# Optimization experiments

Measured on AMD Instinct MI355X. Metric: run time of the kernel, lower is better.

The kernel has to match this reference:

```python
import jax, jax.numpy as jnp
import numpy as np

TIME_GAP_BUCKETS = 64
B, L, H, MAX_T = 256, 200, 256, 256
VOCAB, N_GROUPS = 50000, 16
EPS = 1e-5


def setup_inputs() -> dict:
    key = jax.random.key(0)
    ks = jax.random.split(key, 16)
    lengths = jax.random.randint(ks[0], (B,), 0, L + 1)
    mask = jnp.arange(L)[None, :] < lengths[:, None]

    def toks(k, hi):  # jagged padded-dense: zeros past each row's length
        return jnp.where(mask, jax.random.randint(k, (B, L), 0, hi), 0)

    inp = {
        'history_tokens': toks(ks[1], VOCAB),
        'history_post_tokens': toks(ks[2], VOCAB),
        'history_author_tokens': toks(ks[3], VOCAB),
        'history_action_tokens': toks(ks[4], VOCAB),
        'history_time_gap': toks(ks[5], TIME_GAP_BUCKETS + 1),
        'history_group_ids': jnp.where(mask, jnp.sort(jax.random.randint(ks[6], (B, L), 1, N_GROUPS + 1), axis=1), 0),
        'lengths': lengths,
    }
    s = 0.02
    inp['token_emb'] = jax.random.normal(ks[7], (VOCAB, H)) * s
    inp['ln_gamma'] = jnp.ones((6 * H,))
    inp['ln_beta'] = jnp.zeros((6 * H,))
    inp['w1'] = jax.random.normal(ks[8], (6 * H, 4 * H)) * (1.0 / np.sqrt(6 * H)).astype(np.float32)
    inp['b1'] = jnp.zeros((4 * H,))
    inp['w2'] = jax.random.normal(ks[9], (4 * H, H)) * (1.0 / np.sqrt(4 * H)).astype(np.float32)
    inp['b2'] = jnp.zeros((H,))
    inp['time_gap_emb'] = (jax.random.normal(ks[10], (TIME_GAP_BUCKETS + 1, H)) * s).at[0].set(0.0)  # padding_idx=0
    inp['group_emb'] = (jax.random.normal(ks[11], (N_GROUPS + 1, H)) * s).at[0].set(0.0)  # padding_idx=0
    inp['pos_emb'] = jax.random.normal(ks[12], (MAX_T, H)) * s
    inp['sep_token'] = jax.random.normal(ks[13], (H,)) * 0.02
    return inp


def _layernorm(x, g, b):
    mu = jnp.mean(x, axis=-1, keepdims=True)
    var = jnp.mean(jnp.square(x - mu), axis=-1, keepdims=True)
    return (x - mu) * jax.lax.rsqrt(var + EPS) * g + b


def _merge_with_sep(event_tokens, group_ids, mask, sep_token):
    # mask is a prefix mask (positions < lengths), so valid tokens are contiguous.
    Bn, Ln, Hn = event_tokens.shape
    next_mask = jnp.pad(mask[:, 1:], ((0, 0), (0, 1)))
    next_group = jnp.pad(group_ids[:, 1:], ((0, 0), (0, 1)))
    sep_after = mask & next_mask & (group_ids != next_group)  # insert sep after token i
    seps_before = jnp.cumsum(sep_after, axis=1) - sep_after.astype(jnp.int32)  # exclusive scan
    token_pos = jnp.arange(Ln)[None, :] + seps_before  # position within merged piece list
    total = mask.sum(axis=1) + sep_after.sum(axis=1)  # [B] merged piece count
    offset = MAX_T - total  # right-align; negative -> leading pieces dropped
    tok_idx = offset[:, None] + token_pos
    sep_idx = tok_idx + 1
    tok_idx = jnp.where(mask & (tok_idx >= 0), tok_idx, MAX_T)  # MAX_T => dropped
    sep_idx = jnp.where(sep_after & (sep_idx >= 0), sep_idx, MAX_T)
    sep_rows = jnp.broadcast_to(sep_token, (Ln, Hn))

    def scatter_one(ev, ti, si):
        buf = jnp.zeros((MAX_T, Hn), ev.dtype)
        buf = buf.at[ti].set(ev, mode='drop')
        buf = buf.at[si].set(sep_rows, mode='drop')
        return buf

    merged = jax.vmap(scatter_one)(event_tokens, tok_idx, sep_idx)
    merged_len = jnp.minimum(total, MAX_T)
    merged_mask = jnp.arange(MAX_T)[None, :] >= (MAX_T - merged_len)[:, None]
    return merged, merged_mask


def reference(history_tokens, history_post_tokens, history_author_tokens,
              history_action_tokens, history_time_gap, history_group_ids,
              lengths, token_emb, ln_gamma, ln_beta, w1, b1, w2, b2,
              time_gap_emb, group_emb, pos_emb, sep_token):
    mask = jnp.arange(L)[None, :] < lengths[:, None]
    hh = token_emb[history_tokens]
    ph = token_emb[history_post_tokens]
    ah = token_emb[history_author_tokens]
    ch = token_emb[history_action_tokens]
    th = time_gap_emb[jnp.clip(history_time_gap, 0, TIME_GAP_BUCKETS)]
    gh = group_emb[history_group_ids]
    ev = jnp.concatenate([hh, ph, ah, ch, th, gh], axis=-1)  # [B, L, 6H]
    x = _layernorm(ev, ln_gamma, ln_beta)
    x = jax.nn.silu(x @ w1 + b1)  # dropout is identity in eval mode
    event_tokens = x @ w2 + b2  # [B, L, H]
    merged, mm = _merge_with_sep(event_tokens, history_group_ids, mask, sep_token)
    merged = (merged + pos_emb[None]) * mm[..., None].astype(merged.dtype)
    return merged, mm
```

## Files before the change

### kernel.cpp

```cpp
#include <hip/hip_runtime.h>
#include <hip/hip_bf16.h>
#include <math.h>

#define B_    256
#define L_    200
#define H_    256
#define MAXT  256
#define SIXH  1536
#define FOURH 1024
#define NPOS  (B_ * L_)

typedef __attribute__((ext_vector_type(8))) short short8;
typedef __attribute__((ext_vector_type(4))) float f32x4;

typedef __attribute__((address_space(3))) void lds_void;
typedef const __attribute__((address_space(1))) void gbl_void;

#define ASM_BAR() asm volatile("s_barrier" ::: "memory")
#define VMCNT3()  asm volatile("s_waitcnt vmcnt(3)" ::: "memory")
#define VMCNT0()  asm volatile("s_waitcnt vmcnt(0)" ::: "memory")

__global__ void scan_offsets(const int* __restrict__ lengths,
                             int* __restrict__ offsets) {
  int t = threadIdx.x;
  int lane = t & 63, wv = t >> 6;
  int len = lengths[t];
  int s = len;
#pragma unroll
  for (int o = 1; o < 64; o <<= 1) {
    int v = __shfl_up(s, o);
    if (lane >= o) s += v;
  }
  __shared__ int wsum[4];
  if (lane == 63) wsum[wv] = s;
  __syncthreads();
  int pre = 0;
#pragma unroll
  for (int k = 0; k < 4; k++)
    if (k < wv) pre += wsum[k];
  s += pre;
  offsets[t] = s - len;
  if (t == 255) offsets[B_] = s;
}

__global__ void zero_pad_x(__hip_bfloat16* __restrict__ x,
                           const int* __restrict__ offsets) {
  int total = offsets[B_];
  int padded = (total + 255) & ~255;
  int row = total + blockIdx.x;
  if (row >= padded) return;
  int t = threadIdx.x;
#pragma unroll
  for (int j = 0; j < 6; j++)
    x[(size_t)row * SIXH + j * 256 + t] = __float2bfloat16(0.0f);
}

__global__ void tpos_kernel(const int* __restrict__ gids,
                            const int* __restrict__ lengths,
                            const int* __restrict__ offsets,
                            int* __restrict__ tpos) {
  int b = blockIdx.x, t = threadIdx.x;
  __shared__ int g[L_];
  int len = lengths[b];
  for (int l = t; l < len; l += 64) g[l] = gids[b * L_ + l];
  __syncthreads();
  if (t != 0) return;
  int base = offsets[b];
  int nsep = 0;
  for (int l = 0; l + 1 < len; l++)
    if (g[l] != g[l + 1]) nsep++;
  int total = len + nsep;
  int off = MAXT - total;
  int sb = 0;
  for (int l = 0; l < len; l++) {
    int ti = off + l + sb;
    tpos[base + l] = (ti >= 0) ? (b * MAXT + ti) : -1;
    if (l + 1 < len && g[l] != g[l + 1]) sb++;
  }
}

__global__ void transpose_both(const float* __restrict__ w1,
                               __hip_bfloat16* __restrict__ w1t,
                               const float* __restrict__ w2,
                               __hip_bfloat16* __restrict__ w2t) {
  __shared__ float tile[32][33];
  int id = blockIdx.x;
  const float* in; __hip_bfloat16* out; int R, C, tc, tr;
  if (id < 1536) {
    in = w1; out = w1t; R = 1536; C = 1024; tc = id & 31; tr = id >> 5;
  } else {
    int j = id - 1536;
    in = w2; out = w2t; R = 1024; C = 256; tc = j & 7; tr = j >> 3;
  }
  int tx = threadIdx.x & 31, ty = threadIdx.x >> 5;
#pragma unroll
  for (int i = 0; i < 4; i++)
    tile[ty + i * 8][tx] = in[(size_t)(tr * 32 + ty + i * 8) * C + tc * 32 + tx];
  __syncthreads();
#pragma unroll
  for (int i = 0; i < 4; i++)
    out[(size_t)(tc * 32 + ty + i * 8) * R + tr * 32 + tx] =
        __float2bfloat16(tile[tx][ty + i * 8]);
}

__global__ void embed_ln_kernel(const int* __restrict__ tok0,
                                const int* __restrict__ tok1,
                                const int* __restrict__ tok2,
                                const int* __restrict__ tok3,
                                const int* __restrict__ tgap,
                                const int* __restrict__ gid,
                                const int* __restrict__ lengths,
                                const int* __restrict__ offsets,
                                const float* __restrict__ token_emb,
                                const float* __restrict__ tg_emb,
                                const float* __restrict__ g_emb,
                                const float* __restrict__ gamma,
                                const float* __restrict__ beta,
                                __hip_bfloat16* __restrict__ xout) {
  int l = blockIdx.x, b = blockIdx.y;
  if (l >= lengths[b]) return;
  int pos = b * L_ + l;
  int row = offsets[b] + l;
  int t = threadIdx.x;
  int wv = t >> 6;
  int ln = t & 63;
  int c4 = ln * 4;

  const float* tab;
  int idx;
  if (wv == 0)      { tab = token_emb; idx = tok0[pos]; }
  else if (wv == 1) { tab = token_emb; idx = tok1[pos]; }
  else if (wv == 2) { tab = token_emb; idx = tok2[pos]; }
  else if (wv == 3) { tab = token_emb; idx = tok3[pos]; }
  else if (wv == 4) { tab = tg_emb;    idx = min(max(tgap[pos], 0), 64); }
  else              { tab = g_emb;     idx = gid[pos]; }

  float4 v = *(const float4*)&tab[(size_t)idx * H_ + c4];

  float s = v.x + v.y + v.z + v.w;
  float q = v.x * v.x + v.y * v.y + v.z * v.z + v.w * v.w;
#pragma unroll
  for (int o = 32; o; o >>= 1) { s += __shfl_down(s, o); q += __shfl_down(q, o); }
  __shared__ float ps[6], pq[6];
  if (ln == 0) { ps[wv] = s; pq[wv] = q; }
  __syncthreads();
  float ts = 0.f, tq = 0.f;
#pragma unroll
  for (int k = 0; k < 6; k++) { ts += ps[k]; tq += pq[k]; }
  float mu = ts * (1.0f / 1536.0f);
  float var = tq * (1.0f / 1536.0f) - mu * mu;
  float rstd = rsqrtf(var + 1e-5f);

  int cbase = wv * 256 + c4;
  float4 gm = *(const float4*)&gamma[cbase];
  float4 bt = *(const float4*)&beta[cbase];
  float y0 = (v.x - mu) * rstd * gm.x + bt.x;
  float y1 = (v.y - mu) * rstd * gm.y + bt.y;
  float y2 = (v.z - mu) * rstd * gm.z + bt.z;
  float y3 = (v.w - mu) * rstd * gm.w + bt.w;
  __hip_bfloat16 h0 = __float2bfloat16(y0), h1 = __float2bfloat16(y1);
  __hip_bfloat16 h2 = __float2bfloat16(y2), h3 = __float2bfloat16(y3);
  ushort4 pk;
  pk.x = *(unsigned short*)&h0; pk.y = *(unsigned short*)&h1;
  pk.z = *(unsigned short*)&h2; pk.w = *(unsigned short*)&h3;
  *(ushort4*)&xout[(size_t)row * SIXH + cbase] = pk;
}

__global__ __launch_bounds__(512, 4)
void gemm1_bk32(const __hip_bfloat16* __restrict__ A,
                const __hip_bfloat16* __restrict__ Bt,
                const float* __restrict__ bias,
                __hip_bfloat16* __restrict__ out,
                const int* __restrict__ total_ptr) {
  constexpr int K = SIXH;
  constexpr int NS = K / 32;
  constexpr int N = FOURH;

  __shared__ __align__(16) char lds[49152];

  int total = total_ptr[0];
  int padded = (total + 255) & ~255;
  int num_mt = padded >> 8;

  int flat = blockIdx.y * 8 + blockIdx.x;
  int xcd = flat & 7;
  int j = flat >> 3;
  int nt = j & 7;
  int mt = (j >> 3) * 8 + xcd;
  if (mt >= num_mt) return;
  int m0 = mt * 256;
  int n0 = nt * 128;

  int tid = threadIdx.x;
  int lane = tid & 63;
  int w = tid >> 6;
  int wave_m = w >> 1;
  int wave_n = w & 1;

  int r15 = lane & 15, g = lane >> 4;
  int slot_r = (((r15 & 1) << 2) | g) ^ (r15 >> 1);
  int lane_off = (r15 >> 1) * 128 + slot_r * 16;

  int s0 = (tid & 7) ^ ((tid >> 3) & 7);
  int scol = (s0 & 3) * 8;
  int row0 = ((tid >> 3) << 1) + (s0 >> 2);

  float bv4[4];
#pragma unroll
  for (int ni = 0; ni < 4; ni++)
    bv4[ni] = bias[n0 + wave_n * 64 + ni * 16 + r15];

#define AREG(d) (lds + (d) * 16384)
#define BREG(d) (lds + 32768 + (d) * 8192)

#define STAGE_A(ks, d)                                                         \
  do {                                                                         \
    __builtin_amdgcn_global_load_lds(                                          \
        (gbl_void*)(A + (size_t)(m0 + row0) * K + (ks) * 32 + scol),           \
        (lds_void*)(AREG(d) + (size_t)tid * 16 % 8192 + 0 * 8192 +             \
                    (tid * 16 / 8192) * 0),                                    \
        16, 0, 0);                                                             \
  } while (0)
#undef STAGE_A
#define STAGE_A(ks, d)                                                         \
  do {                                                                         \
    __builtin_amdgcn_global_load_lds(                                          \
        (gbl_void*)(A + (size_t)(m0 + row0) * K + (ks) * 32 + scol),           \
        (lds_void*)(AREG(d) + w * 1024), 16, 0, 0);                            \
    __builtin_amdgcn_global_load_lds(                                          \
        (gbl_void*)(A + (size_t)(m0 + row0 + 128) * K + (ks) * 32 + scol),     \
        (lds_void*)(AREG(d) + 8192 + w * 1024), 16, 0, 0);                     \
  } while (0)
#define STAGE_B(ks, d)                                                         \
  __builtin_amdgcn_global_load_lds(                                            \
      (gbl_void*)(Bt + (size_t)(n0 + row0) * K + (ks) * 32 + scol),            \
      (lds_void*)(BREG(d) + w * 1024), 16, 0, 0)

  f32x4 acc[4][4] = {};

  STAGE_A(0, 0); STAGE_B(0, 0);
  STAGE_A(1, 1); STAGE_B(1, 1);
  VMCNT3();
  ASM_BAR();

  for (int ks = 0; ks < NS; ++ks) {
    int d = ks & 1;
    int kn = (ks + 2 < NS) ? ks + 2 : NS - 1;
    char* Ad = AREG(d);
    char* Bd = BREG(d);

    short8 a[4], b[4];
#pragma unroll
    for (int ni = 0; ni < 4; ni++)
      b[ni] = *(const short8*)(Bd + (wave_n * 64 + ni * 16) * 64 + lane_off);
#pragma unroll
    for (int mi = 0; mi < 4; mi++)
      a[mi] = *(const short8*)(Ad + (wave_m * 64 + mi * 16) * 64 + lane_off);
    ASM_BAR();

    STAGE_A(kn, d); STAGE_B(kn, d);

    __builtin_amdgcn_s_setprio(1);
#pragma unroll
    for (int mi = 0; mi < 4; mi++)
#pragma unroll
      for (int ni = 0; ni < 4; ni++)
        acc[mi][ni] = __builtin_amdgcn_mfma_f32_16x16x32_bf16(a[mi], b[ni],
                                                              acc[mi][ni], 0, 0, 0);
    __builtin_amdgcn_s_setprio(0);

    VMCNT3();
    ASM_BAR();
  }
  VMCNT0();

  int r0 = g * 4;
#pragma unroll
  for (int mi = 0; mi < 4; mi++)
#pragma unroll
    for (int ni = 0; ni < 4; ni++) {
      int col = n0 + wave_n * 64 + ni * 16 + r15;
      float bv = bv4[ni];
#pragma unroll
      for (int r = 0; r < 4; r++) {
        int row = m0 + wave_m * 64 + mi * 16 + r0 + r;
        float v = acc[mi][ni][r] + bv;
        v = v / (1.0f + __expf(-v));
        out[(size_t)row * N + col] = __float2bfloat16(v);
      }
    }
#undef STAGE_A
#undef STAGE_B
#undef AREG
#undef BREG
}

__global__ void gemm2_scatter(const __hip_bfloat16* __restrict__ A,
                              const __hip_bfloat16* __restrict__ Bt,
                              const float* __restrict__ bias,
                              const int* __restrict__ tpos,
                              const float* __restrict__ pos_emb,
                              float* __restrict__ out,
                              const int* __restrict__ total_ptr,
                              int N, int K) {
  int m0 = blockIdx.y * 128;
  int total = total_ptr[0];
  int padded = (total + 127) & ~127;
  if (m0 >= padded) return;

  __shared__ __hip_bfloat16 As[128 * 64];
  __shared__ __hip_bfloat16 Bs[128 * 64];
  int n0 = blockIdx.x * 128;
  int tid = threadIdx.x;
  int lane = tid & 63, wid = tid >> 6;
  int wm = (wid >> 1) * 64, wn = (wid & 1) * 64;

  int srow = (lane >> 3);
  int scol = (lane & 7) * 8;

  f32x4 acc[4][4] = {};

  for (int k0 = 0; k0 < K; k0 += 64) {
#pragma unroll
    for (int i = 0; i < 4; i++) {
      int c = wid * 4 + i;
      int row = c * 8 + srow;
      __builtin_amdgcn_global_load_lds(
          (gbl_void*)&A[(size_t)(m0 + row) * K + k0 + scol],
          (lds_void*)(As + c * 512), 16, 0, 0);
      __builtin_amdgcn_global_load_lds(
          (gbl_void*)&Bt[(size_t)(n0 + row) * K + k0 + scol],
          (lds_void*)(Bs + c * 512), 16, 0, 0);
    }
    __syncthreads();
#pragma unroll
    for (int kk = 0; kk < 64; kk += 32) {
      short8 a[4], bb[4];
#pragma unroll
      for (int m = 0; m < 4; m++)
        a[m] = *(const short8*)&As[(wm + m * 16 + (lane & 15)) * 64 + kk +
                                   8 * (lane >> 4)];
#pragma unroll
      for (int n = 0; n < 4; n++)
        bb[n] = *(const short8*)&Bs[(wn + n * 16 + (lane & 15)) * 64 + kk +
                                    8 * (lane >> 4)];
#pragma unroll
      for (int m = 0; m < 4; m++)
#pragma unroll
        for (int n = 0; n < 4; n++)
          acc[m][n] = __builtin_amdgcn_mfma_f32_16x16x32_bf16(a[m], bb[n],
                                                              acc[m][n], 0, 0, 0);
    }
    __syncthreads();
  }

  int r0 = (lane >> 4) * 4;
  int cc = lane & 15;
#pragma unroll
  for (int m = 0; m < 4; m++) {
#pragma unroll
    for (int r = 0; r < 4; r++) {
      int row = m0 + wm + m * 16 + r0 + r;
      if (row >= total) continue;
      int pa = tpos[row];
      if (pa < 0) continue;
      int p = pa & (MAXT - 1);
#pragma unroll
      for (int n = 0; n < 4; n++) {
        int col = n0 + wn + n * 16 + cc;
        float v = acc[m][n][r] + bias[col] + pos_emb[p * H_ + col];
        out[(size_t)pa * H_ + col] = v;
      }
    }
  }
}

__global__ void merge2_kernel(const int* __restrict__ gids,
                              const int* __restrict__ lengths,
                              const float* __restrict__ sep_token,
                              const float* __restrict__ pos_emb,
                              float* __restrict__ out) {
  int b = blockIdx.x, t = threadIdx.x;
  __shared__ signed char src[MAXT];
  __shared__ int g[L_];
  __shared__ int sh_total;
  int len = lengths[b];
  src[t] = 0;
  for (int l = t; l < len; l += 256) g[l] = gids[b * L_ + l];
  __syncthreads();
  if (t == 0) {
    int nsep = 0;
    for (int l = 0; l + 1 < len; l++)
      if (g[l] != g[l + 1]) nsep++;
    int total = len + nsep;
    sh_total = total;
    int off = MAXT - total;
    int sb = 0;
    for (int l = 0; l < len; l++) {
      int ti = off + l + sb;
      if (ti >= 0) src[ti] = 2;
      if (l + 1 < len && g[l] != g[l + 1]) {
        if (ti + 1 >= 0) src[ti + 1] = 1;
        sb++;
      }
    }
  }
  __syncthreads();
  int total = sh_total;
  int mlen = min(total, MAXT);

  int q = t >> 6, lane = t & 63, c4 = lane * 4;
  float4 sep4 = *(const float4*)&sep_token[c4];
  float* orow = out + (size_t)b * MAXT * H_;
  for (int p0 = 0; p0 < MAXT; p0 += 4) {
    int p = p0 + q;
    int s = src[p];
    if (s == 2) continue;
    float4 v;
    if (s == 1) {
      float4 pe = *(const float4*)&pos_emb[p * H_ + c4];
      v.x = sep4.x + pe.x; v.y = sep4.y + pe.y;
      v.z = sep4.z + pe.z; v.w = sep4.w + pe.w;
    } else {
      v.x = 0.f; v.y = 0.f; v.z = 0.f; v.w = 0.f;
    }
    *(float4*)&orow[(size_t)p * H_ + c4] = v;
  }
  float* mm = out + (size_t)B_ * MAXT * H_;
  mm[b * MAXT + t] = (t >= MAXT - mlen) ? 1.0f : 0.0f;
}

extern "C" void kernel_launch(void* const* d_in, const int* in_sizes, int n_in,
                              void* d_out, int out_size, void* d_ws,
                              size_t ws_size, hipStream_t stream) {
  const int* tok0 = (const int*)d_in[0];
  const int* tok1 = (const int*)d_in[1];
  const int* tok2 = (const int*)d_in[2];
  const int* tok3 = (const int*)d_in[3];
  const int* tgap = (const int*)d_in[4];
  const int* gid  = (const int*)d_in[5];
  const int* lengths = (const int*)d_in[6];
  const float* token_emb = (const float*)d_in[7];
  const float* gamma = (const float*)d_in[8];
  const float* beta  = (const float*)d_in[9];
  const float* w1 = (const float*)d_in[10];
  const float* b1 = (const float*)d_in[11];
  const float* w2 = (const float*)d_in[12];
  const float* b2 = (const float*)d_in[13];
  const float* tg_emb = (const float*)d_in[14];
  const float* g_emb  = (const float*)d_in[15];
  const float* pos_emb = (const float*)d_in[16];
  const float* sep_tok = (const float*)d_in[17];

  const size_t NEEDED = 265815044;
  if (ws_size < NEEDED) return;

  char* ws = (char*)d_ws;
  __hip_bfloat16* x = (__hip_bfloat16*)ws;
  int* tpos = (int*)ws;
  __hip_bfloat16* h = (__hip_bfloat16*)(ws + 157286400);
  __hip_bfloat16* w1t = (__hip_bfloat16*)(ws + 262144000);
  __hip_bfloat16* w2t = (__hip_bfloat16*)(ws + 265289728);
  int* offsets = (int*)(ws + 265814016);

  scan_offsets<<<1, 256, 0, stream>>>(lengths, offsets);
  zero_pad_x<<<256, 256, 0, stream>>>(x, offsets);

  transpose_both<<<1792, 256, 0, stream>>>(w1, w1t, w2, w2t);

  embed_ln_kernel<<<dim3(L_, B_), 384, 0, stream>>>(
      tok0, tok1, tok2, tok3, tgap, gid, lengths, offsets, token_emb, tg_emb,
      g_emb, gamma, beta, x);

  gemm1_bk32<<<dim3(8, NPOS / 256), 512, 0, stream>>>(x, w1t, b1, h,
                                                      offsets + B_);

  tpos_kernel<<<B_, 64, 0, stream>>>(gid, lengths, offsets, tpos);

  gemm2_scatter<<<dim3(H_ / 128, NPOS / 128), 256, 0, stream>>>(
      h, w2t, b2, tpos, pos_emb, (float*)d_out, offsets + B_, H_, FOURH);

  merge2_kernel<<<B_, 256, 0, stream>>>(gid, lengths, sep_tok, pos_emb,
                                        (float*)d_out);
}
```

Measured before the change: 257.2 us.

## Use three-stage LDS ring buffer in gemm1 to drop mid-iteration barrier

The first GEMM's double-buffered LDS staging becomes a triple-buffered ring, growing LDS from 48 KB to 72 KB. Because the stage being refilled is never the one being read, the barrier between the LDS fragment reads and the next global->LDS prefetch is removed, leaving one barrier per K-step. The last two K-steps are peeled out so no redundant loads are issued. The larger LDS footprint may reduce the number of blocks resident per CU.

```diff
diff --git a/kernel.cpp b/kernel.cpp
--- a/kernel.cpp
+++ b/kernel.cpp
@@ -167,7 +167,7 @@
 }
 
 __global__ __launch_bounds__(512, 4)
-void gemm1_bk32(const __hip_bfloat16* __restrict__ A,
+void gemm1_ring(const __hip_bfloat16* __restrict__ A,
                 const __hip_bfloat16* __restrict__ Bt,
                 const float* __restrict__ bias,
                 __hip_bfloat16* __restrict__ out,
@@ -176,7 +176,7 @@
   constexpr int NS = K / 32;
   constexpr int N = FOURH;
 
-  __shared__ __align__(16) char lds[49152];
+  __shared__ __align__(16) char lds[73728];
 
   int total = total_ptr[0];
   int padded = (total + 255) & ~255;
@@ -210,44 +210,37 @@
   for (int ni = 0; ni < 4; ni++)
     bv4[ni] = bias[n0 + wave_n * 64 + ni * 16 + r15];
 
-#define AREG(d) (lds + (d) * 16384)
-#define BREG(d) (lds + 32768 + (d) * 8192)
-
-#define STAGE_A(ks, d)                                                         \
+  const char* gA0 = (const char*)(A + (size_t)(m0 + row0) * K + scol);
+  const char* gA1 = (const char*)(A + (size_t)(m0 + row0 + 128) * K + scol);
+  const char* gB  = (const char*)(Bt + (size_t)(n0 + row0) * K + scol);
+
+#define STAGE_AT(kb, aoff, boff)                                               \
   do {                                                                         \
+    __builtin_amdgcn_global_load_lds((gbl_void*)(gA0 + (kb)),                  \
+                                     (lds_void*)(lds + (aoff) + w * 1024),     \
+                                     16, 0, 0);                                \
     __builtin_amdgcn_global_load_lds(                                          \
-        (gbl_void*)(A + (size_t)(m0 + row0) * K + (ks) * 32 + scol),           \
-        (lds_void*)(AREG(d) + (size_t)tid * 16 % 8192 + 0 * 8192 +             \
-                    (tid * 16 / 8192) * 0),                                    \
+        (gbl_void*)(gA1 + (kb)), (lds_void*)(lds + (aoff) + 8192 + w * 1024),  \
+        16, 0, 0);                                                             \
+    __builtin_amdgcn_global_load_lds(                                          \
+        (gbl_void*)(gB + (kb)), (lds_void*)(lds + 49152 + (boff) + w * 1024),  \
         16, 0, 0);                                                             \
   } while (0)
-#undef STAGE_A
-#define STAGE_A(ks, d)                                                         \
-  do {                                                                         \
-    __builtin_amdgcn_global_load_lds(                                          \
-        (gbl_void*)(A + (size_t)(m0 + row0) * K + (ks) * 32 + scol),           \
-        (lds_void*)(AREG(d) + w * 1024), 16, 0, 0);                            \
-    __builtin_amdgcn_global_load_lds(                                          \
-        (gbl_void*)(A + (size_t)(m0 + row0 + 128) * K + (ks) * 32 + scol),     \
-        (lds_void*)(AREG(d) + 8192 + w * 1024), 16, 0, 0);                     \
-  } while (0)
-#define STAGE_B(ks, d)                                                         \
-  __builtin_amdgcn_global_load_lds(                                            \
-      (gbl_void*)(Bt + (size_t)(n0 + row0) * K + (ks) * 32 + scol),            \
-      (lds_void*)(BREG(d) + w * 1024), 16, 0, 0)
 
   f32x4 acc[4][4] = {};
 
-  STAGE_A(0, 0); STAGE_B(0, 0);
-  STAGE_A(1, 1); STAGE_B(1, 1);
+  STAGE_AT(0, 0, 0);
+  STAGE_AT(64, 16384, 8192);
   VMCNT3();
   ASM_BAR();
 
-  for (int ks = 0; ks < NS; ++ks) {
-    int d = ks & 1;
-    int kn = (ks + 2 < NS) ? ks + 2 : NS - 1;
-    char* Ad = AREG(d);
-    char* Bd = BREG(d);
+  int rdA = 0, rdB = 0;
+  int stA = 32768, stB = 16384;
+  int kb = 128;
+
+  for (int ks = 0; ks < NS - 2; ++ks) {
+    char* Ad = lds + rdA;
+    char* Bd = lds + 49152 + rdB;
 
     short8 a[4], b[4];
 #pragma unroll
@@ -256,9 +249,8 @@
 #pragma unroll
     for (int mi = 0; mi < 4; mi++)
       a[mi] = *(const short8*)(Ad + (wave_m * 64 + mi * 16) * 64 + lane_off);
-    ASM_BAR();
-
-    STAGE_A(kn, d); STAGE_B(kn, d);
+
+    STAGE_AT(kb, stA, stB);
 
     __builtin_amdgcn_s_setprio(1);
 #pragma unroll
@@ -271,8 +263,52 @@
 
     VMCNT3();
     ASM_BAR();
-  }
-  VMCNT0();
+
+    kb += 64;
+    rdA = (rdA == 32768) ? 0 : rdA + 16384;
+    rdB = (rdB == 16384) ? 0 : rdB + 8192;
+    stA = (stA == 32768) ? 0 : stA + 16384;
+    stB = (stB == 16384) ? 0 : stB + 8192;
+  }
+
+  {
+    char* Ad = lds + rdA;
+    char* Bd = lds + 49152 + rdB;
+    short8 a[4], b[4];
+#pragma unroll
+    for (int ni = 0; ni < 4; ni++)
+      b[ni] = *(const short8*)(Bd + (wave_n * 64 + ni * 16) * 64 + lane_off);
+#pragma unroll
+    for (int mi = 0; mi < 4; mi++)
+      a[mi] = *(const short8*)(Ad + (wave_m * 64 + mi * 16) * 64 + lane_off);
+#pragma unroll
+    for (int mi = 0; mi < 4; mi++)
+#pragma unroll
+      for (int ni = 0; ni < 4; ni++)
+        acc[mi][ni] = __builtin_amdgcn_mfma_f32_16x16x32_bf16(a[mi], b[ni],
+                                                              acc[mi][ni], 0, 0, 0);
+    VMCNT0();
+    ASM_BAR();
+    rdA = (rdA == 32768) ? 0 : rdA + 16384;
+    rdB = (rdB == 16384) ? 0 : rdB + 8192;
+  }
+  {
+    char* Ad = lds + rdA;
+    char* Bd = lds + 49152 + rdB;
+    short8 a[4], b[4];
+#pragma unroll
+    for (int ni = 0; ni < 4; ni++)
+      b[ni] = *(const short8*)(Bd + (wave_n * 64 + ni * 16) * 64 + lane_off);
+#pragma unroll
+    for (int mi = 0; mi < 4; mi++)
+      a[mi] = *(const short8*)(Ad + (wave_m * 64 + mi * 16) * 64 + lane_off);
+#pragma unroll
+    for (int mi = 0; mi < 4; mi++)
+#pragma unroll
+      for (int ni = 0; ni < 4; ni++)
+        acc[mi][ni] = __builtin_amdgcn_mfma_f32_16x16x32_bf16(a[mi], b[ni],
+                                                              acc[mi][ni], 0, 0, 0);
+  }
 
   int r0 = g * 4;
 #pragma unroll
@@ -289,10 +325,7 @@
         out[(size_t)row * N + col] = __float2bfloat16(v);
       }
     }
-#undef STAGE_A
-#undef STAGE_B
-#undef AREG
-#undef BREG
+#undef STAGE_AT
 }
 
 __global__ void gemm2_scatter(const __hip_bfloat16* __restrict__ A,
@@ -472,7 +505,7 @@
       tok0, tok1, tok2, tok3, tgap, gid, lengths, offsets, token_emb, tg_emb,
       g_emb, gamma, beta, x);
 
-  gemm1_bk32<<<dim3(8, NPOS / 256), 512, 0, stream>>>(x, w1t, b1, h,
+  gemm1_ring<<<dim3(8, NPOS / 256), 512, 0, stream>>>(x, w1t, b1, h,
                                                       offsets + B_);
 
   tpos_kernel<<<B_, 64, 0, stream>>>(gid, lengths, offsets, tpos);
```

Result: no change. 258.0 us (+0.3%).
